# Performance work log

Measured on AMD Instinct MI355X. Metric: run time of the kernel, lower is better.

Reference implementation:

```python
import jax, jax.numpy as jnp
import numpy as np

B, L, D, T = 2, 2048, 1536, 2
INITRANGE = 0.1

def setup_inputs() -> dict:
    key = jax.random.key(0)
    k1, k2 = jax.random.split(key)
    hidden_states = jax.random.normal(k1, (B, L, D), dtype=jnp.float32)
    # decoder: Linear(2*D, T) with uniform(-0.1, 0.1) weight, zero bias
    W = jax.random.uniform(k2, (T, 2 * D), dtype=jnp.float32, minval=-INITRANGE, maxval=INITRANGE)
    b = jnp.zeros((T,), dtype=jnp.float32)
    return {"hidden_states": hidden_states, "W": W, "b": b}

def reference(hidden_states, W, b):
    # Faithful fused version of:
    #   prod = h[:,:,None,:] * h[:,None,:,:]; diff = h[:,:,None,:] - h[:,None,:,:]
    #   logits = cat(prod, diff, -1) @ W.T + b
    # Split W into the product half and the difference half.
    d = hidden_states.shape[-1]
    Wp, Wd = W[:, :d], W[:, d:]                      # [T, D] each
    # prod term: sum_d h[b,i,d] * h[b,j,d] * Wp[t,d]
    hw = jnp.einsum('bid,td->btid', hidden_states, Wp)          # [B,T,L,D]
    prod_logits = jnp.einsum('btid,bjd->bijt', hw, hidden_states)  # [B,L,L,T]
    # diff term: (h[b,i]-h[b,j]) @ Wd.T = (h@Wd.T)[b,i] - (h@Wd.T)[b,j]
    hd = jnp.einsum('bid,td->bit', hidden_states, Wd)           # [B,L,T]
    diff_logits = hd[:, :, None, :] - hd[:, None, :, :]         # [B,L,L,T]
    logits = prod_logits + diff_logits + b
    # symmetrize over the (i, j) pair axes
    logits = (logits + jnp.transpose(logits, (0, 2, 1, 3))) * 0.5
    return logits
```

## Files before the change

### kernel.cpp

```cpp
#include <hip/hip_runtime.h>
#include <hip/hip_bf16.h>
#include <stdint.h>

#define B_ 2
#define L_ 2048
#define D_ 1536

typedef __attribute__((ext_vector_type(4))) float  f32x4;
typedef __attribute__((ext_vector_type(8))) __bf16 bf16x8;

__device__ __forceinline__ unsigned short f2bf(float f) {
  unsigned int u = __float_as_uint(f);
  u += 0x7fffu + ((u >> 16) & 1u);
  return (unsigned short)(u >> 16);
}

__global__ __launch_bounds__(256) void conv_kernel(
    const float* __restrict__ hs, const float* __restrict__ W,
    unsigned short* __restrict__ X, unsigned short* __restrict__ P) {
  const int idx  = blockIdx.x * 256 + threadIdx.x;
  const int base = idx * 4;
  const int d    = base % D_;
  const float4 h  = *(const float4*)(hs + base);
  const float4 w0 = *(const float4*)(W + d);
  const float4 w1 = *(const float4*)(W + 2 * D_ + d);
  ushort4 x, p0, p1;
  x.x  = f2bf(h.x);        x.y  = f2bf(h.y);        x.z  = f2bf(h.z);        x.w  = f2bf(h.w);
  p0.x = f2bf(h.x * w0.x); p0.y = f2bf(h.y * w0.y); p0.z = f2bf(h.z * w0.z); p0.w = f2bf(h.w * w0.w);
  p1.x = f2bf(h.x * w1.x); p1.y = f2bf(h.y * w1.y); p1.z = f2bf(h.z * w1.z); p1.w = f2bf(h.w * w1.w);
  *(ushort4*)(X + base) = x;
  *(ushort4*)(P + base) = p0;
  *(ushort4*)(P + (size_t)B_ * L_ * D_ + base) = p1;
}

__device__ __forceinline__ void async16(const void* g, const void* l) {
  __builtin_amdgcn_global_load_lds(
      (const __attribute__((address_space(1))) void*)g,
      (__attribute__((address_space(3))) void*)l, 16, 0, 0);
}

__global__ __launch_bounds__(256, 2) void gemm_kernel(
    const unsigned short* __restrict__ X, const unsigned short* __restrict__ P,
    const float* __restrict__ bias, float2* __restrict__ out) {
  __shared__ unsigned short As0[2 * 128 * 32];
  __shared__ unsigned short As1[2 * 128 * 32];
  __shared__ unsigned short Bs [2 * 128 * 32];

  const int tid = threadIdx.x;

  const int id     = blockIdx.x;
  const int xcd    = id & 7;
  const int u      = id >> 3;
  const int within = u & 15;
  const int pp     = u >> 4;
  const int Pp     = pp * 8 + xcd;
  const int bz     = Pp >> 4;
  const int pr     = Pp & 15;
  const int I0     = ((pr >> 2) * 4 + (within >> 2)) * 128;
  const int J0     = ((pr & 3)  * 4 + (within & 3))  * 128;

  const int srow = tid >> 2;
  const int cs   = tid & 3;
  const int gc   = cs ^ ((srow >> 1) & 3);
  const int scol = gc * 8;
  const int ldst = tid * 8;

  const size_t planeB = (size_t)B_ * L_ * D_;
  const unsigned short* pA0 = P + ((size_t)(bz * L_ + I0 + srow)) * D_ + scol;
  const unsigned short* pA1 = pA0 + planeB;
  const unsigned short* pB  = X + ((size_t)(bz * L_ + J0 + srow)) * D_ + scol;

  const int lane = tid & 63;
  const int w    = tid >> 6;
  const int wi   = (w & 1) * 64;
  const int wj   = (w >> 1) * 64;
  const int lr   = lane & 15;
  const int q    = lane >> 4;
  const int ccol = (q ^ ((lr >> 1) & 3)) * 8;

  int aoff[4], boff[4];
#pragma unroll
  for (int m = 0; m < 4; ++m) {
    aoff[m] = (wi + m * 16 + lr) * 32 + ccol;
    boff[m] = (wj + m * 16 + lr) * 32 + ccol;
  }

  f32x4 acc0[4][4] = {};
  f32x4 acc1[4][4] = {};

#define STAGE(buf, koff)                                              \
  do {                                                                \
    async16(pA0 + (koff),           As0 + (buf) * 4096 + ldst);       \
    async16(pA0 + (koff) + 64 * D_, As0 + (buf) * 4096 + ldst + 2048);\
    async16(pA1 + (koff),           As1 + (buf) * 4096 + ldst);       \
    async16(pA1 + (koff) + 64 * D_, As1 + (buf) * 4096 + ldst + 2048);\
    async16(pB  + (koff),           Bs  + (buf) * 4096 + ldst);       \
    async16(pB  + (koff) + 64 * D_, Bs  + (buf) * 4096 + ldst + 2048);\
  } while (0)

  STAGE(0, 0);
  for (int k = 0; k < D_ / 32; ++k) {
    __syncthreads();
    if (k < D_ / 32 - 1) STAGE((k + 1) & 1, (k + 1) * 32);
    const unsigned short* A0b = As0 + (k & 1) * 4096;
    const unsigned short* A1b = As1 + (k & 1) * 4096;
    const unsigned short* Bb  = Bs  + (k & 1) * 4096;
    bf16x8 a0f[4], a1f[4], bf_[4];
#pragma unroll
    for (int m = 0; m < 4; ++m) {
      a0f[m] = *(const bf16x8*)(A0b + aoff[m]);
      a1f[m] = *(const bf16x8*)(A1b + aoff[m]);
    }
#pragma unroll
    for (int n = 0; n < 4; ++n) bf_[n] = *(const bf16x8*)(Bb + boff[n]);
#pragma unroll
    for (int m = 0; m < 4; ++m)
#pragma unroll
      for (int n = 0; n < 4; ++n) {
        acc0[m][n] = __builtin_amdgcn_mfma_f32_16x16x32_bf16(a0f[m], bf_[n], acc0[m][n], 0, 0, 0);
        acc1[m][n] = __builtin_amdgcn_mfma_f32_16x16x32_bf16(a1f[m], bf_[n], acc1[m][n], 0, 0, 0);
      }
  }
#undef STAGE

  const float bias0 = bias[0], bias1 = bias[1];
#pragma unroll
  for (int m = 0; m < 4; ++m) {
#pragma unroll
    for (int r = 0; r < 4; ++r) {
      const int i = I0 + wi + m * 16 + q * 4 + r;
      float2* orow = out + (size_t)(bz * L_ + i) * L_ + (J0 + wj + lr);
#pragma unroll
      for (int n = 0; n < 4; ++n) {
        float2 v;
        v.x = acc0[m][n][r] + bias0;
        v.y = acc1[m][n][r] + bias1;
        orow[n * 16] = v;
      }
    }
  }
}

extern "C" void kernel_launch(void* const* d_in, const int* in_sizes, int n_in,
                              void* d_out, int out_size, void* d_ws, size_t ws_size,
                              hipStream_t stream) {
  const float* hs   = (const float*)d_in[0];
  const float* W    = (const float*)d_in[1];
  const float* bias = (const float*)d_in[2];

  unsigned short* X = (unsigned short*)d_ws;
  unsigned short* P = X + (size_t)B_ * L_ * D_;

  const int nconv = (B_ * L_ * D_ / 4) / 256;
  conv_kernel<<<nconv, 256, 0, stream>>>(hs, W, X, P);

  gemm_kernel<<<512, 256, 0, stream>>>(X, P, bias, (float2*)d_out);
}
```

Measured before the change: 150.9 us.

## Replace direct-to-LDS async loads with register-staged double-buffered prefetch

The GEMM main loop no longer loads tiles straight into LDS with global_load_lds. It loads them into two sets of registers, writes them to LDS with regular stores, and unrolls the K loop by two so that one register set is in flight while the other buffer is being computed. The aim is to hide global-memory latency behind the MFMA work and to let the compiler schedule the loads more freely. In exchange it adds 48 VGPRs of staging registers on top of large accumulators and extra LDS write instructions, which risks spills or lower occupancy under launch_bounds(256,2).

Measured after the change: 141.7 us. -6.1%, faster.

```diff
diff --git a/kernel.cpp b/kernel.cpp
--- a/kernel.cpp
+++ b/kernel.cpp
@@ -31,12 +31,6 @@
   *(ushort4*)(X + base) = x;
   *(ushort4*)(P + base) = p0;
   *(ushort4*)(P + (size_t)B_ * L_ * D_ + base) = p1;
-}
-
-__device__ __forceinline__ void async16(const void* g, const void* l) {
-  __builtin_amdgcn_global_load_lds(
-      (const __attribute__((address_space(1))) void*)g,
-      (__attribute__((address_space(3))) void*)l, 16, 0, 0);
 }
 
 __global__ __launch_bounds__(256, 2) void gemm_kernel(
@@ -88,40 +82,72 @@
   f32x4 acc0[4][4] = {};
   f32x4 acc1[4][4] = {};
 
-#define STAGE(buf, koff)                                              \
-  do {                                                                \
-    async16(pA0 + (koff),           As0 + (buf) * 4096 + ldst);       \
-    async16(pA0 + (koff) + 64 * D_, As0 + (buf) * 4096 + ldst + 2048);\
-    async16(pA1 + (koff),           As1 + (buf) * 4096 + ldst);       \
-    async16(pA1 + (koff) + 64 * D_, As1 + (buf) * 4096 + ldst + 2048);\
-    async16(pB  + (koff),           Bs  + (buf) * 4096 + ldst);       \
-    async16(pB  + (koff) + 64 * D_, Bs  + (buf) * 4096 + ldst + 2048);\
+  uint4 ra0l, ra0h, ra1l, ra1h, rbl, rbh;
+  uint4 sa0l, sa0h, sa1l, sa1h, sbl, sbh;
+
+#define GLOAD0(koff)                                      \
+  do {                                                    \
+    ra0l = *(const uint4*)(pA0 + (koff));                 \
+    ra0h = *(const uint4*)(pA0 + (koff) + 64 * D_);       \
+    ra1l = *(const uint4*)(pA1 + (koff));                 \
+    ra1h = *(const uint4*)(pA1 + (koff) + 64 * D_);       \
+    rbl  = *(const uint4*)(pB  + (koff));                 \
+    rbh  = *(const uint4*)(pB  + (koff) + 64 * D_);       \
+  } while (0)
+#define GLOAD1(koff)                                      \
+  do {                                                    \
+    sa0l = *(const uint4*)(pA0 + (koff));                 \
+    sa0h = *(const uint4*)(pA0 + (koff) + 64 * D_);       \
+    sa1l = *(const uint4*)(pA1 + (koff));                 \
+    sa1h = *(const uint4*)(pA1 + (koff) + 64 * D_);       \
+    sbl  = *(const uint4*)(pB  + (koff));                 \
+    sbh  = *(const uint4*)(pB  + (koff) + 64 * D_);       \
+  } while (0)
+#define DSW(buf, A0L, A0H, A1L, A1H, BL, BH)              \
+  do {                                                    \
+    *(uint4*)(As0 + (buf) * 4096 + ldst)        = A0L;    \
+    *(uint4*)(As0 + (buf) * 4096 + ldst + 2048) = A0H;    \
+    *(uint4*)(As1 + (buf) * 4096 + ldst)        = A1L;    \
+    *(uint4*)(As1 + (buf) * 4096 + ldst + 2048) = A1H;    \
+    *(uint4*)(Bs  + (buf) * 4096 + ldst)        = BL;     \
+    *(uint4*)(Bs  + (buf) * 4096 + ldst + 2048) = BH;     \
+  } while (0)
+#define COMPUTE(buf)                                                           \
+  do {                                                                         \
+    const unsigned short* A0b = As0 + (buf) * 4096;                            \
+    const unsigned short* A1b = As1 + (buf) * 4096;                            \
+    const unsigned short* Bb  = Bs  + (buf) * 4096;                            \
+    bf16x8 a0f[4], a1f[4], bf_[4];                                             \
+    _Pragma("unroll") for (int m = 0; m < 4; ++m) {                            \
+      a0f[m] = *(const bf16x8*)(A0b + aoff[m]);                                \
+      a1f[m] = *(const bf16x8*)(A1b + aoff[m]);                                \
+    }                                                                          \
+    _Pragma("unroll") for (int n = 0; n < 4; ++n)                              \
+      bf_[n] = *(const bf16x8*)(Bb + boff[n]);                                 \
+    _Pragma("unroll") for (int m = 0; m < 4; ++m)                              \
+      _Pragma("unroll") for (int n = 0; n < 4; ++n) {                          \
+        acc0[m][n] = __builtin_amdgcn_mfma_f32_16x16x32_bf16(a0f[m], bf_[n],   \
+                                                             acc0[m][n], 0, 0, 0); \
+        acc1[m][n] = __builtin_amdgcn_mfma_f32_16x16x32_bf16(a1f[m], bf_[n],   \
+                                                             acc1[m][n], 0, 0, 0); \
+      }                                                                        \
   } while (0)
 
-  STAGE(0, 0);
-  for (int k = 0; k < D_ / 32; ++k) {
+  GLOAD0(0);
+  for (int k = 0; k < D_ / 32; k += 2) {
+    DSW(0, ra0l, ra0h, ra1l, ra1h, rbl, rbh);
+    GLOAD1((k + 1) * 32);
     __syncthreads();
-    if (k < D_ / 32 - 1) STAGE((k + 1) & 1, (k + 1) * 32);
-    const unsigned short* A0b = As0 + (k & 1) * 4096;
-    const unsigned short* A1b = As1 + (k & 1) * 4096;
-    const unsigned short* Bb  = Bs  + (k & 1) * 4096;
-    bf16x8 a0f[4], a1f[4], bf_[4];
-#pragma unroll
-    for (int m = 0; m < 4; ++m) {
-      a0f[m] = *(const bf16x8*)(A0b + aoff[m]);
-      a1f[m] = *(const bf16x8*)(A1b + aoff[m]);
-    }
-#pragma unroll
-    for (int n = 0; n < 4; ++n) bf_[n] = *(const bf16x8*)(Bb + boff[n]);
-#pragma unroll
-    for (int m = 0; m < 4; ++m)
-#pragma unroll
-      for (int n = 0; n < 4; ++n) {
-        acc0[m][n] = __builtin_amdgcn_mfma_f32_16x16x32_bf16(a0f[m], bf_[n], acc0[m][n], 0, 0, 0);
-        acc1[m][n] = __builtin_amdgcn_mfma_f32_16x16x32_bf16(a1f[m], bf_[n], acc1[m][n], 0, 0, 0);
-      }
+    COMPUTE(0);
+    DSW(1, sa0l, sa0h, sa1l, sa1h, sbl, sbh);
+    if (k + 2 < D_ / 32) GLOAD0((k + 2) * 32);
+    __syncthreads();
+    COMPUTE(1);
   }
-#undef STAGE
+#undef GLOAD0
+#undef GLOAD1
+#undef DSW
+#undef COMPUTE
 
   const float bias0 = bias[0], bias1 = bias[1];
 #pragma unroll
```
